# Optimization experiments

Hardware: AMD Instinct MI355X
Metric: run time of the kernel (lower is better)

Reference implementation:

```python
import jax, jax.numpy as jnp
import numpy as np


def setup_inputs() -> dict:
    key = jax.random.key(0)
    k1, k2, k3, k4 = jax.random.split(key, 4)
    N, F, E, M = 50000, 128, 1600000, 1024
    return {
        "molec_feature_vectures": jax.random.normal(k1, (N, F), dtype=jnp.float32),
        "W": jax.random.normal(k2, (F, F), dtype=jnp.float32),
        "mo_neighbour_indices": jax.random.randint(k3, (2, E), 0, N, dtype=jnp.int64),
        "mo_mol_id": jax.random.randint(k4, (E,), 0, M, dtype=jnp.int64),
        "n_output": M,
    }


def reference(molec_feature_vectures, W, mo_neighbour_indices, mo_mol_id, n_output):
    # Gather endpoint features for each neighbor pair: [E, F]
    fi = molec_feature_vectures[mo_neighbour_indices[0]]
    fj = molec_feature_vectures[mo_neighbour_indices[1]]
    # Symmetric bilinear form (mode='pes'): s_n = fi_n . (W + W^T) . fj_n
    Ws = W + W.T  # [F, F]
    # Fuse as (fi @ Ws) * fj summed over F to avoid a 3-operand einsum blowup
    scalars = jnp.einsum('ni,ij,nj->n', fi, Ws, fj)  # [E]
    # Segment-sum per molecule
    res = jax.ops.segment_sum(scalars, mo_mol_id, num_segments=n_output)  # [M]
    return res
```

## Files before the change

### kernel.cpp

```cpp
#include <hip/hip_runtime.h>
#include <hip/hip_bf16.h>

#define FDIM 128
#define BROWS 32
#define NBLK 128

typedef __attribute__((ext_vector_type(8))) short short8v;
typedef __attribute__((ext_vector_type(4))) float f32x4;
typedef __attribute__((ext_vector_type(2))) _Float16 half2v;

static __device__ __forceinline__ unsigned short f2bf(float x) {
    unsigned u = __float_as_uint(x);
    unsigned r = 0x7fffu + ((u >> 16) & 1u);
    return (unsigned short)((u + r) >> 16);
}
static __device__ __forceinline__ float bf2f(unsigned short h) {
    return __uint_as_float((unsigned)h << 16);
}
static __device__ __forceinline__ void split2(float v, short& h, short& l) {
    unsigned short hh = f2bf(v);
    h = (short)hh;
    l = (short)f2bf(v - bf2f(hh));
}

static __device__ __forceinline__ half2v u2h(unsigned u) {
    union { unsigned u; half2v h; } c; c.u = u; return c.h;
}
static __device__ __forceinline__ unsigned pack2h(float a, float b) {
    union { unsigned u; half2v h; } c;
    c.h[0] = (_Float16)a; c.h[1] = (_Float16)b; return c.u;
}
static __device__ __forceinline__ unsigned short f2h(float x) {
    union { unsigned short s; _Float16 h; } c; c.h = (_Float16)x; return c.s;
}
static __device__ __forceinline__ float fdot2(half2v a, half2v b, float c) {
#if defined(__has_builtin) && __has_builtin(__builtin_amdgcn_fdot2)
    return __builtin_amdgcn_fdot2(a, b, c, false);
#else
    return fmaf((float)a[1], (float)b[1], fmaf((float)a[0], (float)b[0], c));
#endif
}

__global__ __launch_bounds__(512, 4) void gemm_mfma(
    const float* __restrict__ Fm, const float* __restrict__ W,
    unsigned short* __restrict__ Gh, int N) {
    __shared__ __align__(16) unsigned short sH[128 * 136];
    __shared__ __align__(16) unsigned short sL[128 * 136];

    for (int idx = threadIdx.x; idx < 128 * 128; idx += 512) {
        int i = idx >> 7, j = idx & 127;
        float w = W[idx] + W[j * 128 + i];
        short h, l;
        split2(w, h, l);
        sH[i * 136 + j] = (unsigned short)h;
        sL[i * 136 + j] = (unsigned short)l;
    }
    __syncthreads();

    const int wid  = threadIdx.x >> 6;
    const int lane = threadIdx.x & 63;
    const int ar   = lane & 15;
    const int kg   = lane >> 4;
    const int row0 = blockIdx.x * 128 + wid * 16;
    const int gr   = row0 + ar;
    const bool rv  = gr < N;
    const float* fp = Fm + (size_t)gr * FDIM;

    f32x4 acc[8];
#pragma unroll
    for (int t = 0; t < 8; ++t) acc[t] = (f32x4){0.f, 0.f, 0.f, 0.f};

#pragma unroll
    for (int ks = 0; ks < 4; ++ks) {
        const int k0 = ks * 32 + kg * 8;
        float4 fa = make_float4(0.f, 0.f, 0.f, 0.f);
        float4 fb = make_float4(0.f, 0.f, 0.f, 0.f);
        if (rv) {
            fa = *(const float4*)(fp + k0);
            fb = *(const float4*)(fp + k0 + 4);
        }
        short8v ah, al;
        {
            short h, l;
            split2(fa.x, h, l); ah[0] = h; al[0] = l;
            split2(fa.y, h, l); ah[1] = h; al[1] = l;
            split2(fa.z, h, l); ah[2] = h; al[2] = l;
            split2(fa.w, h, l); ah[3] = h; al[3] = l;
            split2(fb.x, h, l); ah[4] = h; al[4] = l;
            split2(fb.y, h, l); ah[5] = h; al[5] = l;
            split2(fb.z, h, l); ah[6] = h; al[6] = l;
            split2(fb.w, h, l); ah[7] = h; al[7] = l;
        }
#pragma unroll
        for (int ct = 0; ct < 8; ++ct) {
            const short8v bh = *(const short8v*)(sH + (ct * 16 + ar) * 136 + k0);
            const short8v bl = *(const short8v*)(sL + (ct * 16 + ar) * 136 + k0);
            acc[ct] = __builtin_amdgcn_mfma_f32_16x16x32_bf16(ah, bh, acc[ct], 0, 0, 0);
            acc[ct] = __builtin_amdgcn_mfma_f32_16x16x32_bf16(ah, bl, acc[ct], 0, 0, 0);
            acc[ct] = __builtin_amdgcn_mfma_f32_16x16x32_bf16(al, bh, acc[ct], 0, 0, 0);
        }
    }

#pragma unroll
    for (int r = 0; r < 4; ++r) {
        const int orow = row0 + kg * 4 + r;
        if (orow < N) {
#pragma unroll
            for (int ct = 0; ct < 8; ++ct)
                Gh[(size_t)orow * FDIM + ct * 16 + ar] = f2h(acc[ct][r]);
        }
    }
}

__global__ __launch_bounds__(1024) void k_hist(const int* __restrict__ idx, int E,
                                               int nb, unsigned* __restrict__ M,
                                               float* __restrict__ out, int Mout) {
    if (blockIdx.x == 0) {
        for (int i = threadIdx.x; i < Mout; i += 1024) out[i] = 0.f;
    }
    extern __shared__ unsigned cnt[];
    for (int i = threadIdx.x; i < nb; i += 1024) cnt[i] = 0;
    __syncthreads();
    int chunk = (E + NBLK - 1) / NBLK;
    int s = blockIdx.x * chunk;
    int e_end = min(E, s + chunk);
    for (int e = s + threadIdx.x; e < e_end; e += 1024) {
        int i1 = idx[E + e];
        atomicAdd(&cnt[i1 >> 5], 1u);
    }
    __syncthreads();
    for (int i = threadIdx.x; i < nb; i += 1024)
        M[(size_t)blockIdx.x * nb + i] = cnt[i];
}

__global__ __launch_bounds__(256) void k_mscan2(unsigned* __restrict__ M, int nb,
                                                unsigned* __restrict__ tot) {
    int b = blockIdx.x * 4 + (threadIdx.x >> 6);
    int lane = threadIdx.x & 63;
    if (b >= nb) return;
    unsigned m0 = M[(size_t)(2 * lane + 0) * nb + b];
    unsigned m1 = M[(size_t)(2 * lane + 1) * nb + b];
    unsigned s = m0 + m1;
    unsigned incl = s;
#pragma unroll
    for (int d = 1; d < 64; d <<= 1) {
        unsigned u = __shfl_up(incl, d, 64);
        if (lane >= d) incl += u;
    }
    unsigned run = incl - s;
    M[(size_t)(2 * lane + 0) * nb + b] = run; run += m0;
    M[(size_t)(2 * lane + 1) * nb + b] = run;
    if (lane == 63) tot[b] = incl;
}

__global__ __launch_bounds__(256) void k_bscan(const unsigned* __restrict__ tot, int nb,
                                               unsigned* __restrict__ bucketStart) {
    __shared__ unsigned wS[4];
    int t = threadIdx.x;
    unsigned v0, v1, v2, v3, v4, v5, v6, v7;
    int b0 = t * 8;
    v0 = (b0 + 0 < nb) ? tot[b0 + 0] : 0u;
    v1 = (b0 + 1 < nb) ? tot[b0 + 1] : 0u;
    v2 = (b0 + 2 < nb) ? tot[b0 + 2] : 0u;
    v3 = (b0 + 3 < nb) ? tot[b0 + 3] : 0u;
    v4 = (b0 + 4 < nb) ? tot[b0 + 4] : 0u;
    v5 = (b0 + 5 < nb) ? tot[b0 + 5] : 0u;
    v6 = (b0 + 6 < nb) ? tot[b0 + 6] : 0u;
    v7 = (b0 + 7 < nb) ? tot[b0 + 7] : 0u;
    unsigned l0 = 0, l1 = v0, l2 = l1 + v1, l3 = l2 + v2, l4 = l3 + v3,
             l5 = l4 + v4, l6 = l5 + v5, l7 = l6 + v6;
    unsigned s = l7 + v7;
    int lane = t & 63, wid = t >> 6;
    unsigned incl = s;
    for (int d = 1; d < 64; d <<= 1) {
        unsigned u = __shfl_up(incl, d, 64);
        if (lane >= d) incl += u;
    }
    if (lane == 63) wS[wid] = incl;
    __syncthreads();
    unsigned wOff = 0;
    for (int i = 0; i < wid; ++i) wOff += wS[i];
    unsigned base = wOff + incl - s;
    if (b0 + 0 < nb) bucketStart[b0 + 0] = base + l0;
    if (b0 + 1 < nb) bucketStart[b0 + 1] = base + l1;
    if (b0 + 2 < nb) bucketStart[b0 + 2] = base + l2;
    if (b0 + 3 < nb) bucketStart[b0 + 3] = base + l3;
    if (b0 + 4 < nb) bucketStart[b0 + 4] = base + l4;
    if (b0 + 5 < nb) bucketStart[b0 + 5] = base + l5;
    if (b0 + 6 < nb) bucketStart[b0 + 6] = base + l6;
    if (b0 + 7 < nb) bucketStart[b0 + 7] = base + l7;
    if (t == 255) bucketStart[nb] = base + s;
}

__global__ __launch_bounds__(1024) void k_scatter(const int* __restrict__ idx,
                                                  const int* __restrict__ mol, int E,
                                                  int nb, const unsigned* __restrict__ M,
                                                  const unsigned* __restrict__ bucketStart,
                                                  unsigned* __restrict__ sortedE) {
    extern __shared__ unsigned cur[];
    for (int i = threadIdx.x; i < nb; i += 1024)
        cur[i] = M[(size_t)blockIdx.x * nb + i] + bucketStart[i];
    __syncthreads();
    int chunk = (E + NBLK - 1) / NBLK;
    int s = blockIdx.x * chunk;
    int e_end = min(E, s + chunk);
    for (int e = s + threadIdx.x; e < e_end; e += 1024) {
        int i0 = idx[e];
        int i1 = idx[E + e];
        int m  = mol[e];
        int b  = i1 >> 5;
        int loc = i1 & 31;
        unsigned pos = atomicAdd(&cur[b], 1u);
        sortedE[pos] = (unsigned)i0 | ((unsigned)m << 16) | ((unsigned)loc << 26);
    }
}

__global__ __launch_bounds__(512, 6) void edge_kernel(
    const unsigned short* __restrict__ Gh, const float* __restrict__ Fm,
    const unsigned* __restrict__ sortedE, const unsigned* __restrict__ bucketStart,
    float* __restrict__ out, int N, int Mout) {
    __shared__ __align__(16) unsigned short sFrow[BROWS * FDIM];
    __shared__ float smol[1024];

    const int b = blockIdx.x;
    const int row0 = b * BROWS;
    const int nrow = min(BROWS, N - row0);

    for (int k = threadIdx.x; k < nrow * 16; k += 512) {
        int r = k >> 4, g = k & 15;
        const float4* src = (const float4*)(Fm + (size_t)(row0 + r) * FDIM + g * 8);
        float4 v0 = src[0], v1 = src[1];
        uint4 u;
        u.x = pack2h(v0.x, v0.y);
        u.y = pack2h(v0.z, v0.w);
        u.z = pack2h(v1.x, v1.y);
        u.w = pack2h(v1.z, v1.w);
        *(uint4*)(sFrow + r * FDIM + g * 8) = u;
    }
    for (int i = threadIdx.x; i < 1024; i += 512) smol[i] = 0.f;
    __syncthreads();

    const int s = (int)bucketStart[b];
    const int e_end = (int)bucketStart[b + 1];
    const int lane = threadIdx.x & 63;
    const int sub  = lane >> 4;
    const int t16  = lane & 15;
    const int off16 = t16 * 8;
    const int wid  = threadIdx.x >> 6;

#define DOT8(p, g, f) \
    p = fdot2(u2h((g).x), u2h((f).x), p); \
    p = fdot2(u2h((g).y), u2h((f).y), p); \
    p = fdot2(u2h((g).z), u2h((f).z), p); \
    p = fdot2(u2h((g).w), u2h((f).w), p);

    int base = s + wid * 16;
    unsigned pk0 = 0u, pk1 = 0u, pk2 = 0u, pk3 = 0u;
    if (base + sub < e_end)      pk0 = sortedE[base + sub];
    if (base + 4 + sub < e_end)  pk1 = sortedE[base + 4 + sub];
    if (base + 8 + sub < e_end)  pk2 = sortedE[base + 8 + sub];
    if (base + 12 + sub < e_end) pk3 = sortedE[base + 12 + sub];

    while (base < e_end) {
        const int nbase = base + 128;
        unsigned npk0 = 0u, npk1 = 0u, npk2 = 0u, npk3 = 0u;
        if (nbase + sub < e_end)      npk0 = sortedE[nbase + sub];
        if (nbase + 4 + sub < e_end)  npk1 = sortedE[nbase + 4 + sub];
        if (nbase + 8 + sub < e_end)  npk2 = sortedE[nbase + 8 + sub];
        if (nbase + 12 + sub < e_end) npk3 = sortedE[nbase + 12 + sub];

        const uint4 g0 = *(const uint4*)(Gh + (size_t)(pk0 & 0xffffu) * FDIM + off16);
        const uint4 g1 = *(const uint4*)(Gh + (size_t)(pk1 & 0xffffu) * FDIM + off16);
        const uint4 g2 = *(const uint4*)(Gh + (size_t)(pk2 & 0xffffu) * FDIM + off16);
        const uint4 g3 = *(const uint4*)(Gh + (size_t)(pk3 & 0xffffu) * FDIM + off16);
        const uint4 f0 = *(const uint4*)(sFrow + (pk0 >> 26) * FDIM + off16);
        const uint4 f1 = *(const uint4*)(sFrow + (pk1 >> 26) * FDIM + off16);
        const uint4 f2 = *(const uint4*)(sFrow + (pk2 >> 26) * FDIM + off16);
        const uint4 f3 = *(const uint4*)(sFrow + (pk3 >> 26) * FDIM + off16);

        float p0 = 0.f, p1 = 0.f, p2 = 0.f, p3 = 0.f;
        DOT8(p0, g0, f0);
        DOT8(p1, g1, f1);
        DOT8(p2, g2, f2);
        DOT8(p3, g3, f3);

        p0 += __shfl_xor(p0, 1, 16);
        p1 += __shfl_xor(p1, 1, 16);
        p2 += __shfl_xor(p2, 1, 16);
        p3 += __shfl_xor(p3, 1, 16);
        p0 += __shfl_xor(p0, 2, 16);
        p1 += __shfl_xor(p1, 2, 16);
        p2 += __shfl_xor(p2, 2, 16);
        p3 += __shfl_xor(p3, 2, 16);
        p0 += __shfl_xor(p0, 4, 16);
        p1 += __shfl_xor(p1, 4, 16);
        p2 += __shfl_xor(p2, 4, 16);
        p3 += __shfl_xor(p3, 4, 16);
        p0 += __shfl_xor(p0, 8, 16);
        p1 += __shfl_xor(p1, 8, 16);
        p2 += __shfl_xor(p2, 8, 16);
        p3 += __shfl_xor(p3, 8, 16);

        if (t16 == 0) {
            if (base + sub < e_end)      atomicAdd(&smol[(pk0 >> 16) & 0x3ff], p0);
            if (base + 4 + sub < e_end)  atomicAdd(&smol[(pk1 >> 16) & 0x3ff], p1);
            if (base + 8 + sub < e_end)  atomicAdd(&smol[(pk2 >> 16) & 0x3ff], p2);
            if (base + 12 + sub < e_end) atomicAdd(&smol[(pk3 >> 16) & 0x3ff], p3);
        }
        pk0 = npk0; pk1 = npk1; pk2 = npk2; pk3 = npk3;
        base = nbase;
    }
#undef DOT8
    __syncthreads();

    for (int i = threadIdx.x; i < Mout; i += 512) {
        float v = smol[i];
        if (v != 0.f) atomicAdd(&out[i], v);
    }
}

extern "C" void kernel_launch(void* const* d_in, const int* in_sizes, int n_in,
                              void* d_out, int out_size, void* d_ws, size_t ws_size,
                              hipStream_t stream) {
    const float* Fm = (const float*)d_in[0];
    const float* W  = (const float*)d_in[1];
    const int* idx  = (const int*)d_in[2];
    const int* mol  = (const int*)d_in[3];
    float* out = (float*)d_out;

    const int N = in_sizes[0] / FDIM;
    const int E = in_sizes[3];

    const int nb = (N + BROWS - 1) / BROWS;

    char* ws = (char*)d_ws;
    size_t o = 0;
    unsigned short* Gh = (unsigned short*)(ws + o);  o += ((size_t)N * FDIM * 2 + 255) & ~(size_t)255;
    unsigned* sortedE = (unsigned*)(ws + o);         o += ((size_t)E * 4 + 255) & ~(size_t)255;
    unsigned* M = (unsigned*)(ws + o);               o += ((size_t)NBLK * nb * 4 + 255) & ~(size_t)255;
    unsigned* tot = (unsigned*)(ws + o);             o += ((size_t)nb * 4 + 255) & ~(size_t)255;
    unsigned* bucketStart = (unsigned*)(ws + o);     o += ((size_t)(nb + 1) * 4 + 255) & ~(size_t)255;

    gemm_mfma<<<(N + 127) / 128, 512, 0, stream>>>(Fm, W, Gh, N);

    size_t smem = (size_t)nb * 4;
    k_hist<<<NBLK, 1024, smem, stream>>>(idx, E, nb, M, out, out_size);
    k_mscan2<<<(nb + 3) / 4, 256, 0, stream>>>(M, nb, tot);
    k_bscan<<<1, 256, 0, stream>>>(tot, nb, bucketStart);
    k_scatter<<<NBLK, 1024, smem, stream>>>(idx, mol, E, nb, M, bucketStart, sortedE);

    edge_kernel<<<nb, 512, 0, stream>>>(Gh, Fm, sortedE, bucketStart, out, N, out_size);
}
```

Before: 209.9 us.

## Replace global output atomics with per-block partials and two-pass reduction; precompute Ws

The edge kernel now writes its per-block molecule sums to a partials buffer instead of issuing global atomicAdds, and two new reduction kernels sum those partials into the output. This also removes the output zeroing from the histogram kernel. Separately, W+W^T and its bf16 hi/lo split are computed once in a small kernel rather than in every GEMM block. The trade is global atomic contention against roughly 6 MB of extra partial writes and reads plus three more kernel launches.

```diff
diff --git a/kernel.cpp b/kernel.cpp
--- a/kernel.cpp
+++ b/kernel.cpp
@@ -4,6 +4,7 @@
 #define FDIM 128
 #define BROWS 32
 #define NBLK 128
+#define NSLICE 32
 
 typedef __attribute__((ext_vector_type(8))) short short8v;
 typedef __attribute__((ext_vector_type(4))) float f32x4;
@@ -41,19 +42,31 @@
 #endif
 }
 
+__global__ void make_ws2(const float* __restrict__ W,
+                         unsigned short* __restrict__ WsH,
+                         unsigned short* __restrict__ WsL) {
+    int idx = blockIdx.x * 256 + threadIdx.x;
+    int i = idx >> 7, j = idx & 127;
+    float w = W[idx] + W[j * 128 + i];
+    short h, l;
+    split2(w, h, l);
+    WsH[idx] = (unsigned short)h;
+    WsL[idx] = (unsigned short)l;
+}
+
 __global__ __launch_bounds__(512, 4) void gemm_mfma(
-    const float* __restrict__ Fm, const float* __restrict__ W,
+    const float* __restrict__ Fm,
+    const unsigned short* __restrict__ WsH, const unsigned short* __restrict__ WsL,
     unsigned short* __restrict__ Gh, int N) {
     __shared__ __align__(16) unsigned short sH[128 * 136];
     __shared__ __align__(16) unsigned short sL[128 * 136];
 
-    for (int idx = threadIdx.x; idx < 128 * 128; idx += 512) {
-        int i = idx >> 7, j = idx & 127;
-        float w = W[idx] + W[j * 128 + i];
-        short h, l;
-        split2(w, h, l);
-        sH[i * 136 + j] = (unsigned short)h;
-        sL[i * 136 + j] = (unsigned short)l;
+    for (int k = threadIdx.x; k < 128 * 16; k += 512) {
+        int i = k >> 4, g = k & 15;
+        *(uint4*)((char*)sH + i * 272 + g * 16) =
+            *(const uint4*)((const char*)WsH + i * 256 + g * 16);
+        *(uint4*)((char*)sL + i * 272 + g * 16) =
+            *(const uint4*)((const char*)WsL + i * 256 + g * 16);
     }
     __syncthreads();
 
@@ -113,11 +126,7 @@
 }
 
 __global__ __launch_bounds__(1024) void k_hist(const int* __restrict__ idx, int E,
-                                               int nb, unsigned* __restrict__ M,
-                                               float* __restrict__ out, int Mout) {
-    if (blockIdx.x == 0) {
-        for (int i = threadIdx.x; i < Mout; i += 1024) out[i] = 0.f;
-    }
+                                               int nb, unsigned* __restrict__ M) {
     extern __shared__ unsigned cnt[];
     for (int i = threadIdx.x; i < nb; i += 1024) cnt[i] = 0;
     __syncthreads();
@@ -218,7 +227,7 @@
 __global__ __launch_bounds__(512, 6) void edge_kernel(
     const unsigned short* __restrict__ Gh, const float* __restrict__ Fm,
     const unsigned* __restrict__ sortedE, const unsigned* __restrict__ bucketStart,
-    float* __restrict__ out, int N, int Mout) {
+    float* __restrict__ part, int N, int Mout) {
     __shared__ __align__(16) unsigned short sFrow[BROWS * FDIM];
     __shared__ float smol[1024];
 
@@ -313,9 +322,32 @@
 #undef DOT8
     __syncthreads();
 
-    for (int i = threadIdx.x; i < Mout; i += 512) {
-        float v = smol[i];
-        if (v != 0.f) atomicAdd(&out[i], v);
+    float* prow = part + (size_t)b * 1024;
+    for (int i = threadIdx.x; i < Mout; i += 512) prow[i] = smol[i];
+}
+
+__global__ __launch_bounds__(256) void k_red1(const float* __restrict__ part, int nb,
+                                              float* __restrict__ partial, int Mout) {
+    int gid = blockIdx.x * 256 + threadIdx.x;
+    int m = gid & 1023;
+    int sl = gid >> 10;
+    int per = (nb + NSLICE - 1) / NSLICE;
+    int b0 = sl * per;
+    int b1 = min(nb, b0 + per);
+    float s = 0.f;
+    if (m < Mout) {
+        for (int b = b0; b < b1; ++b) s += part[(size_t)b * 1024 + m];
+    }
+    partial[sl * 1024 + m] = s;
+}
+
+__global__ __launch_bounds__(256) void k_red2(const float* __restrict__ partial,
+                                              float* __restrict__ out, int Mout) {
+    int m = blockIdx.x * 256 + threadIdx.x;
+    if (m < Mout) {
+        float s = 0.f;
+        for (int sl = 0; sl < NSLICE; ++sl) s += partial[sl * 1024 + m];
+        out[m] = s;
     }
 }
 
@@ -335,19 +367,27 @@
 
     char* ws = (char*)d_ws;
     size_t o = 0;
+    unsigned short* WsH = (unsigned short*)(ws + o); o += 32 * 1024;
+    unsigned short* WsL = (unsigned short*)(ws + o); o += 32 * 1024;
     unsigned short* Gh = (unsigned short*)(ws + o);  o += ((size_t)N * FDIM * 2 + 255) & ~(size_t)255;
     unsigned* sortedE = (unsigned*)(ws + o);         o += ((size_t)E * 4 + 255) & ~(size_t)255;
     unsigned* M = (unsigned*)(ws + o);               o += ((size_t)NBLK * nb * 4 + 255) & ~(size_t)255;
     unsigned* tot = (unsigned*)(ws + o);             o += ((size_t)nb * 4 + 255) & ~(size_t)255;
     unsigned* bucketStart = (unsigned*)(ws + o);     o += ((size_t)(nb + 1) * 4 + 255) & ~(size_t)255;
-
-    gemm_mfma<<<(N + 127) / 128, 512, 0, stream>>>(Fm, W, Gh, N);
+    float* part = (float*)(ws + o);                  o += (size_t)nb * 1024 * sizeof(float);
+    float* partial = (float*)(ws + o);               o += NSLICE * 1024 * sizeof(float);
+
+    make_ws2<<<64, 256, 0, stream>>>(W, WsH, WsL);
+    gemm_mfma<<<(N + 127) / 128, 512, 0, stream>>>(Fm, WsH, WsL, Gh, N);
 
     size_t smem = (size_t)nb * 4;
-    k_hist<<<NBLK, 1024, smem, stream>>>(idx, E, nb, M, out, out_size);
+    k_hist<<<NBLK, 1024, smem, stream>>>(idx, E, nb, M);
     k_mscan2<<<(nb + 3) / 4, 256, 0, stream>>>(M, nb, tot);
     k_bscan<<<1, 256, 0, stream>>>(tot, nb, bucketStart);
     k_scatter<<<NBLK, 1024, smem, stream>>>(idx, mol, E, nb, M, bucketStart, sortedE);
 
-    edge_kernel<<<nb, 512, 0, stream>>>(Gh, Fm, sortedE, bucketStart, out, N, out_size);
-}
+    edge_kernel<<<nb, 512, 0, stream>>>(Gh, Fm, sortedE, bucketStart, part, N, out_size);
+
+    k_red1<<<NSLICE * 4, 256, 0, stream>>>(part, nb, partial, out_size);
+    k_red2<<<(out_size + 255) / 256, 256, 0, stream>>>(partial, out, out_size);
+}
```

Result: faster. 199.1 us (median of 2 runs) (-5.2%).
